# Performance work log

Hardware: AMD Instinct MI355X
Metric: run time of the kernel (lower is better)

## Reference

```python
import jax, jax.numpy as jnp
import numpy as np
from jax import lax

# Geometry constants (mirror ParallelGeometry with angle_ratio=1.0)
PHI_SIZE = 720
T_SIZE = 1024
N = 256            # reco_shape
B = 16             # batch
RHO = float(np.sqrt(2.0))          # ||max_pt - min_pt||/2 for [-1,1]^2
DT = 2.0 * RHO / T_SIZE            # detector step
A = -RHO                           # left edge used in phase factor
DPHI = np.pi / PHI_SIZE            # mean angle step (angle_ratio=1)


def setup_inputs() -> dict:
    key = jax.random.key(0)
    k1, k2, k3 = jax.random.split(key, 3)
    sinos = jax.random.normal(k1, (B, PHI_SIZE, T_SIZE), dtype=jnp.float32)
    kernel_re = jax.random.normal(k2, (T_SIZE // 2 + 1,), dtype=jnp.float32)
    kernel_im = jax.random.normal(k3, (T_SIZE // 2 + 1,), dtype=jnp.float32)
    return {"sinos": sinos, "kernel_re": kernel_re, "kernel_im": kernel_im}


def _filter_sinos(sinos, kernel):
    # fourier_transform (no padding): dt * exp(-i a w) * rfft(sinos)
    omgs = 2.0 * np.pi * jnp.fft.rfftfreq(T_SIZE, d=DT).astype(jnp.float32)  # [T/2+1]
    phase = jnp.exp(-1j * (A * omgs))          # cos(a w) - i sin(a w)
    sino_hat = (DT * phase) * jnp.fft.rfft(sinos, axis=-1)
    filtered_hat = kernel * sino_hat
    # inverse_fourier_transform: exp(+i a w)/dt * filtered_hat, then irfft
    back = (jnp.conj(phase) / DT) * filtered_hat
    return jnp.fft.irfft(back, n=T_SIZE, axis=-1)   # [B, phi, T], real


def _backproject(filtered):
    # Parallel-beam backprojection (ODL RayTransform adjoint):
    # f(x,y) = dphi * sum_phi lin_interp(g[phi], t = x cos(phi) + y sin(phi))
    angles = ((jnp.arange(PHI_SIZE, dtype=jnp.float32) + 0.5) * (np.pi / PHI_SIZE))
    xs = (-1.0 + (jnp.arange(N, dtype=jnp.float32) + 0.5) * (2.0 / N))  # pixel centers
    X, Y = jnp.meshgrid(xs, xs, indexing='ij')      # ODL axis order: [x, y]
    g_seq = jnp.transpose(filtered, (1, 0, 2))      # [phi, B, T]

    def step(acc, inp):
        g, phi = inp                                # g: [B, T]
        t = X * jnp.cos(phi) + Y * jnp.sin(phi)     # [N, N], always in [-rho, rho]
        u = (t + RHO) / DT - 0.5                    # fractional detector index
        i0 = jnp.clip(jnp.floor(u).astype(jnp.int32), 0, T_SIZE - 2)
        w = u - i0.astype(jnp.float32)
        val = g[:, i0] * (1.0 - w) + g[:, i0 + 1] * w   # [B, N, N]
        return acc + val, None

    acc0 = jnp.zeros((filtered.shape[0], N, N), dtype=filtered.dtype)
    acc, _ = lax.scan(step, acc0, (g_seq, angles))
    return acc * jnp.asarray(DPHI, dtype=filtered.dtype)


def reference(sinos, kernel_re, kernel_im):
    kernel = kernel_re.astype(jnp.complex64) + 1j * kernel_im.astype(jnp.complex64)
    filtered = _filter_sinos(sinos, kernel)
    return _backproject(filtered)
```

## Files before the change

kernel.cpp:

```cpp
#include <hip/hip_runtime.h>

#define PHI 720
#define TS 1024
#define NB 16
#define NPIX 256

#define INVDT 362.03867196751236f
#define DXF 0.0078125f
#define DPHI_F 0.0043633231299858237f

#define WS_TW 0
#define WS_ANG 4096
#define WS_PT 8192
#define WS_NEEDED (8192 + 256 * 360 * 16)

__device__ __forceinline__ float2 cmulf2(float2 a, float2 b) {
    return make_float2(a.x * b.x - a.y * b.y, a.x * b.y + a.y * b.x);
}
__device__ __forceinline__ float fract_fast(float x) {
#if __has_builtin(__builtin_amdgcn_fractf)
    return __builtin_amdgcn_fractf(x);
#else
    return x - floorf(x);
#endif
}

__global__ __launch_bounds__(256) void precompute_kernel(char* __restrict__ wsb) {
    const int blk = blockIdx.x, tid = threadIdx.x;
    if (blk < 360) {
        const int e = blk * 256 + tid;
        const unsigned repu = (unsigned)e / 360u;
        const int rep = (int)repu;
        const int a = e - rep * 360;
        const int ti = rep >> 4, tj = rep & 15;
        float s, c;
        sincosf(((float)a + 0.5f) * (3.14159265358979323846f / 720.0f), &s, &c);
        const float x0 = -1.0f + ((float)(ti * 8) + 0.5f) * DXF;
        const float x7 = x0 + 7.0f * DXF;
        const float y0 = -1.0f + ((float)(tj * 8) + 0.5f) * DXF;
        const float y7 = y0 + 7.0f * DXF;
        const float uTmin = (c * x0 + s * y0) * INVDT + 511.5f;
        const float uTmax = (c * x7 + s * y7) * INVDT + 511.5f;
        const float uUmin = (s * x0 - c * y7) * INVDT + 511.5f;
        const float uUmax = (s * x7 - c * y0) * INVDT + 511.5f;
        int wbA = (int)floorf(uTmin - 0.02f) - 1;
        int wbB = (int)floorf(1023.0f - uTmax - 0.02f) - 1;
        int wbC = (int)floorf(uUmin - 0.02f) - 1;
        int wbD = (int)floorf(1023.0f - uUmax - 0.02f) - 1;
        wbA = min(max(wbA, 0), 992);
        wbB = min(max(wbB, 0), 992);
        wbC = min(max(wbC, 0), 992);
        wbD = min(max(wbD, 0), 992);
        uint4 ent;
        ent.x = __float_as_uint(511.5f - (float)wbA);
        ent.y = __float_as_uint(511.5f - (float)wbC);
        ent.z = (unsigned)wbA | ((unsigned)wbB << 16);
        ent.w = (unsigned)wbC | ((unsigned)wbD << 16);
        ((uint4*)(wsb + WS_PT))[e] = ent;
    } else if (blk < 362) {
        const int k = (blk - 360) * 256 + tid;
        float s, c;
        sincosf((float)k * (6.28318530717958647692f / 1024.0f), &s, &c);
        ((float2*)(wsb + WS_TW))[k] = make_float2(c, -s);
    } else {
        const int a = (blk - 362) * 256 + tid;
        if (a < 360) {
            float s, c;
            sincosf(((float)a + 0.5f) * (3.14159265358979323846f / 720.0f), &s, &c);
            ((float2*)(wsb + WS_ANG))[a] = make_float2(c * INVDT, s * INVDT);
        }
    }
}

__device__ __forceinline__ void r4_stage(const float2* __restrict__ s0, float2* __restrict__ d0,
                                         const float2* __restrict__ s1, float2* __restrict__ d1,
                                         const float2* __restrict__ tw, int tid, int m, bool inv) {
    const int q = tid & ~(m - 1);
    const int o = tid + 3 * q;
    float2 w1 = tw[q], w2 = tw[2 * q];
    if (inv) { w1.y = -w1.y; w2.y = -w2.y; }
    #pragma unroll
    for (int f = 0; f < 2; ++f) {
        const float2* s = f ? s1 : s0;
        float2* d = f ? d1 : d0;
        const float2 a = s[tid], b = s[tid + 256], c = s[tid + 512], e = s[tid + 768];
        const float2 A = make_float2(a.x + c.x, a.y + c.y);
        const float2 Bm = cmulf2(w1, make_float2(a.x - c.x, a.y - c.y));
        const float2 C = make_float2(b.x + e.x, b.y + e.y);
        const float2 Dm = cmulf2(w1, make_float2(b.x - e.x, b.y - e.y));
        const float2 D = inv ? make_float2(-Dm.y, Dm.x) : make_float2(Dm.y, -Dm.x);
        d[o]         = make_float2(A.x + C.x, A.y + C.y);
        d[o + m]     = make_float2(Bm.x + D.x, Bm.y + D.y);
        d[o + 2 * m] = cmulf2(w2, make_float2(A.x - C.x, A.y - C.y));
        d[o + 3 * m] = cmulf2(w2, make_float2(Bm.x - D.x, Bm.y - D.y));
    }
}

__device__ __forceinline__ float2 kfac(const float* __restrict__ kr,
                                       const float* __restrict__ ki, int k, float scale) {
    const int kk = (k <= 512) ? k : (1024 - k);
    const float re = kr[kk] * scale;
    float im = ((k == 0) || (k == 512)) ? 0.0f : ki[kk] * scale;
    if (k > 512) im = -im;
    return make_float2(re, im);
}

__global__ __launch_bounds__(256) void filter_fft_kernel(float* __restrict__ sinos,
                                                         const float* __restrict__ kr,
                                                         const float* __restrict__ ki,
                                                         const char* __restrict__ wsb) {
    __shared__ float2 bufA[2][1024];
    __shared__ float2 bufB[2][1024];
    __shared__ float2 tw[512];
    const int tid = threadIdx.x;
    const int wg = blockIdx.x;
    const int lb = (wg & 7) * 360 + (wg >> 3);
    float* base = sinos + (size_t)lb * 4096;

    #pragma unroll
    for (int f = 0; f < 2; ++f) {
        float* r0 = base + f * 2048;
        float* r1 = r0 + 1024;
        #pragma unroll
        for (int h = 0; h < 4; ++h) {
            const int k = tid + h * 256;
            bufA[f][k] = make_float2(r0[k], r1[k]);
        }
    }
    if (wsb) {
        const float2* tg = (const float2*)(wsb + WS_TW);
        tw[tid] = tg[tid];
        tw[tid + 256] = tg[tid + 256];
    } else {
        #pragma unroll
        for (int h = 0; h < 2; ++h) {
            const int k = tid + h * 256;
            float s, c;
            sincosf((float)k * (6.28318530717958647692f / 1024.0f), &s, &c);
            tw[k] = make_float2(c, -s);
        }
    }
    __syncthreads();

    r4_stage(bufA[0], bufB[0], bufA[1], bufB[1], tw, tid, 1, false);   __syncthreads();
    r4_stage(bufB[0], bufA[0], bufB[1], bufA[1], tw, tid, 4, false);   __syncthreads();
    r4_stage(bufA[0], bufB[0], bufA[1], bufB[1], tw, tid, 16, false);  __syncthreads();
    r4_stage(bufB[0], bufA[0], bufB[1], bufA[1], tw, tid, 64, false);  __syncthreads();
    r4_stage(bufA[0], bufB[0], bufA[1], bufB[1], tw, tid, 256, false); __syncthreads();

    {
        const float scale = DPHI_F / 1024.0f;
        const int q = tid;
        const int o = 4 * tid;
        float2 w1 = tw[q], w2 = tw[2 * q];
        w1.y = -w1.y; w2.y = -w2.y;
        const float2 f0 = kfac(kr, ki, tid, scale);
        const float2 f1 = kfac(kr, ki, tid + 256, scale);
        const float2 f2 = kfac(kr, ki, tid + 512, scale);
        const float2 f3 = kfac(kr, ki, tid + 768, scale);
        #pragma unroll
        for (int f = 0; f < 2; ++f) {
            const float2* s = bufB[f];
            float2* d = bufA[f];
            const float2 a = cmulf2(f0, s[tid]);
            const float2 b = cmulf2(f1, s[tid + 256]);
            const float2 c = cmulf2(f2, s[tid + 512]);
            const float2 e = cmulf2(f3, s[tid + 768]);
            const float2 A = make_float2(a.x + c.x, a.y + c.y);
            const float2 Bm = cmulf2(w1, make_float2(a.x - c.x, a.y - c.y));
            const float2 C = make_float2(b.x + e.x, b.y + e.y);
            const float2 Dm = cmulf2(w1, make_float2(b.x - e.x, b.y - e.y));
            const float2 D = make_float2(-Dm.y, Dm.x);
            d[o]     = make_float2(A.x + C.x, A.y + C.y);
            d[o + 1] = make_float2(Bm.x + D.x, Bm.y + D.y);
            d[o + 2] = cmulf2(w2, make_float2(A.x - C.x, A.y - C.y));
            d[o + 3] = cmulf2(w2, make_float2(Bm.x - D.x, Bm.y - D.y));
        }
    }
    __syncthreads();

    r4_stage(bufA[0], bufB[0], bufA[1], bufB[1], tw, tid, 4, true);   __syncthreads();
    r4_stage(bufB[0], bufA[0], bufB[1], bufA[1], tw, tid, 16, true);  __syncthreads();
    r4_stage(bufA[0], bufB[0], bufA[1], bufB[1], tw, tid, 64, true);  __syncthreads();
    r4_stage(bufB[0], bufA[0], bufB[1], bufA[1], tw, tid, 256, true); __syncthreads();

    #pragma unroll
    for (int f = 0; f < 2; ++f) {
        float* r0 = base + f * 2048;
        float* r1 = r0 + 1024;
        #pragma unroll
        for (int h = 0; h < 4; ++h) {
            const int k = tid + h * 256;
            const float2 v = bufA[f][k];
            r0[k] = v.x;
            r1[k] = v.y;
        }
    }
}

__global__ __launch_bounds__(128, 8) void backproj_sym_kernel(const float* __restrict__ filt,
                                                              float* __restrict__ out,
                                                              const char* __restrict__ wsb) {
    __shared__ float lds[2048];
    const int tid = threadIdx.x;
    const int hf = __builtin_amdgcn_readfirstlane(tid >> 6);
    const int l = tid & 63;
    const int wg = blockIdx.x;
    const int lb = ((wg & 7) << 9) | (wg >> 3);
    const int b = lb >> 8;
    const int rep = lb & 255;
    const int ti = rep >> 4, tj = rep & 15;

    const float2* __restrict__ ang = (const float2*)(wsb + WS_ANG);
    const uint4* __restrict__ pt = ((const uint4*)(wsb + WS_PT)) + rep * 360;

    const int ii = l >> 3, jj = l & 7;
    const int ip = ti * 8 + ii, jp = tj * 8 + jj;
    const float Xc = -1.0f + ((float)ip + 0.5f) * DXF;
    const float Yc = -1.0f + ((float)jp + 0.5f) * DXF;
    const int vbyte = ((l & 31) + ((l >> 5) * (360 * 1024))) * 4;
    const float* __restrict__ gb = filt + (size_t)b * (PHI * TS);
    const int lbase = hf * 1024;

    float a0 = 0.f, a1 = 0.f, a2 = 0.f, a3 = 0.f;
    float pf[2][4];

#define STAGE(CH) { \
    _Pragma("unroll") \
    for (int p = 0; p < 2; ++p) { \
        const int ap = hf * 180 + (CH) * 2 + p; \
        const uint4 e = pt[ap]; \
        const char* rp = (const char*)(gb + (ap << 10)); \
        pf[p][0] = *(const float*)(rp + ((e.z & 0xFFFFu) << 2) + vbyte); \
        pf[p][1] = *(const float*)(rp + ((e.z >> 16) << 2) + vbyte); \
        pf[p][2] = *(const float*)(rp + ((e.w & 0xFFFFu) << 2) + vbyte); \
        pf[p][3] = *(const float*)(rp + ((e.w >> 16) << 2) + vbyte); \
    } }

#define WRITE(BUF) { \
    _Pragma("unroll") \
    for (int p = 0; p < 2; ++p) { \
        _Pragma("unroll") \
        for (int w = 0; w < 4; ++w) \
            lds[lbase + (BUF) * 512 + p * 256 + w * 64 + l] = pf[p][w]; \
    } }

#define COMPUTE(BUF, CH) { \
    _Pragma("unroll") \
    for (int p = 0; p < 2; ++p) { \
        const int ap = hf * 180 + (CH) * 2 + p; \
        const uint4 e = pt[ap]; \
        const float2 cs = ang[ap]; \
        const float* slot = &lds[lbase + (BUF) * 512 + p * 256]; \
        const float kFA = __uint_as_float(e.x), kFC = __uint_as_float(e.y); \
        const int wbA = (int)(e.z & 0xFFFFu), wbB = (int)(e.z >> 16); \
        const int wbC = (int)(e.w & 0xFFFFu), wbD = (int)(e.w >> 16); \
        const float uT = fmaf(cs.x, Xc, fmaf(cs.y, Yc, kFA)); \
        const float uU = fmaf(cs.y, Xc, fmaf(cs.x, -Yc, kFC)); \
        const int iA = (int)uT; const float wT = fract_fast(uT); const float oT = 1.0f - wT; \
        const int iC = (int)uU; const float wU = fract_fast(uU); const float oU = 1.0f - wU; \
        const int iB = 1022 - wbA - wbB - iA; \
        const int iD = 1022 - wbC - wbD - iC; \
        { const float g0 = slot[iA],       g1 = slot[iA + 1]; \
          const float h0 = slot[iA + 32],  h1 = slot[iA + 33]; \
          a0 = fmaf(g0, oT, a0); a0 = fmaf(g1, wT, a0); \
          a1 = fmaf(h0, oT, a1); a1 = fmaf(h1, wT, a1); } \
        { const float g0 = slot[64 + iB],  g1 = slot[65 + iB]; \
          const float h0 = slot[96 + iB],  h1 = slot[97 + iB]; \
          a2 = fmaf(g1, oT, a2); a2 = fmaf(g0, wT, a2); \
          a3 = fmaf(h1, oT, a3); a3 = fmaf(h0, wT, a3); } \
        { const float g0 = slot[128 + iC], g1 = slot[129 + iC]; \
          const float h0 = slot[160 + iC], h1 = slot[161 + iC]; \
          a1 = fmaf(g0, oU, a1); a1 = fmaf(g1, wU, a1); \
          a2 = fmaf(h0, oU, a2); a2 = fmaf(h1, wU, a2); } \
        { const float g0 = slot[192 + iD], g1 = slot[193 + iD]; \
          const float h0 = slot[224 + iD], h1 = slot[225 + iD]; \
          a3 = fmaf(g1, oU, a3); a3 = fmaf(g0, wU, a3); \
          a0 = fmaf(h1, oU, a0); a0 = fmaf(h0, wU, a0); } \
    } }

    STAGE(0); WRITE(0);
    for (int cc = 0; cc < 44; ++cc) {
        STAGE(2 * cc + 1);
        COMPUTE(0, 2 * cc);
        WRITE(1);
        STAGE(2 * cc + 2);
        COMPUTE(1, 2 * cc + 1);
        WRITE(0);
    }
    STAGE(89);
    COMPUTE(0, 88);
    WRITE(1);
    COMPUTE(1, 89);

#undef STAGE
#undef WRITE
#undef COMPUTE

    const int bb = b << 8;
    atomicAdd(&out[((size_t)((bb + ip) << 8)) + jp], a0);
    atomicAdd(&out[((size_t)((bb + 255 - jp) << 8)) + ip], a1);
    atomicAdd(&out[((size_t)((bb + 255 - ip) << 8)) + (255 - jp)], a2);
    atomicAdd(&out[((size_t)((bb + jp) << 8)) + (255 - ip)], a3);
}

__global__ __launch_bounds__(256) void backproj_fb_kernel(const float* __restrict__ filt,
                                                          float* __restrict__ out) {
    __shared__ float2 csI[PHI];
    __shared__ float win[8 * 128];
    __shared__ float woffF[8];

    const int tid = threadIdx.x;
    const int wg = blockIdx.x;
    const int lb = ((wg & 7) << 7) | (wg >> 3);
    const int b = lb >> 6;
    const int tile = lb & 63;
    const int i0 = (tile >> 3) * 32;
    const int j0 = (tile & 7) * 32;

    for (int p = tid; p < PHI; p += 256) {
        const float angv = ((float)p + 0.5f) * (float)(3.14159265358979323846 / 720.0);
        float s, c;
        sincosf(angv, &s, &c);
        csI[p] = make_float2(c * INVDT, s * INVDT);
    }

    const int lane = tid & 63;
    const int wv = tid >> 6;
    const int ii = lane & 7;
    const int jj = lane >> 3;
    const int ipx = i0 + ii;
    const int j = j0 + wv * 8 + jj;

    const float Xc = -1.0f + ((float)ipx + 0.5f) * DXF;
    const float Yc = -1.0f + ((float)j + 0.5f) * DXF;

    const int r = tid >> 5;
    const int l32 = tid & 31;
    const float xlo = -1.0f + ((float)i0 + 0.5f) * DXF;
    const float xhi = -1.0f + ((float)i0 + 31.5f) * DXF;
    const float ylo = -1.0f + ((float)j0 + 0.5f) * DXF;
    const float yhi = -1.0f + ((float)j0 + 31.5f) * DXF;

    const float* gb = filt + (size_t)b * PHI * TS;
    float acc0 = 0.f, acc1 = 0.f, acc2 = 0.f, acc3 = 0.f;

    __syncthreads();

    {
        const float2 cs = csI[r];
        const float um = fminf(cs.x * xlo, cs.x * xhi) + fminf(cs.y * ylo, cs.y * yhi) + 511.5f;
        const int wb = (int)floorf(um) - 1;
        const float* grow = gb + (size_t)r * TS;
        #pragma unroll
        for (int h = 0; h < 4; ++h) {
            int gi = wb + l32 + 32 * h;
            gi = gi < 0 ? 0 : (gi > TS - 1 ? TS - 1 : gi);
            win[r * 128 + l32 + 32 * h] = grow[gi];
        }
        if (l32 == 0) woffF[r] = 511.5f + (float)(r * 128 - wb);
    }
    __syncthreads();

    for (int c = 0; c < PHI / 8; ++c) {
        float gp0 = 0.f, gp1 = 0.f, gp2 = 0.f, gp3 = 0.f;
        int wbn = 0;
        const bool more = (c + 1 < PHI / 8);
        if (more) {
            const int a = (c + 1) * 8 + r;
            const float2 cs = csI[a];
            const float um = fminf(cs.x * xlo, cs.x * xhi) + fminf(cs.y * ylo, cs.y * yhi) + 511.5f;
            wbn = (int)floorf(um) - 1;
            const float* grow = gb + (size_t)a * TS;
            int g0 = wbn + l32;      g0 = g0 < 0 ? 0 : (g0 > TS - 1 ? TS - 1 : g0);
            int g1 = wbn + l32 + 32; g1 = g1 < 0 ? 0 : (g1 > TS - 1 ? TS - 1 : g1);
            int g2 = wbn + l32 + 64; g2 = g2 < 0 ? 0 : (g2 > TS - 1 ? TS - 1 : g2);
            int g3 = wbn + l32 + 96; g3 = g3 < 0 ? 0 : (g3 > TS - 1 ? TS - 1 : g3);
            gp0 = grow[g0]; gp1 = grow[g1]; gp2 = grow[g2]; gp3 = grow[g3];
        }
        #pragma unroll
        for (int aa = 0; aa < 8; ++aa) {
            const float2 cs = csI[c * 8 + aa];
            const float offF = woffF[aa];
            float u = fmaf(cs.y, Yc, cs.x * Xc) + offF;
            const float dup = cs.x * 0.0625f;
            #pragma unroll
            for (int p = 0; p < 4; ++p) {
                const int idx = (int)u;
                const float wf = fract_fast(u);
                const float g0 = win[idx], g1 = win[idx + 1];
                if (p == 0) acc0 = fmaf(wf, g1 - g0, acc0 + g0);
                else if (p == 1) acc1 = fmaf(wf, g1 - g0, acc1 + g0);
                else if (p == 2) acc2 = fmaf(wf, g1 - g0, acc2 + g0);
                else acc3 = fmaf(wf, g1 - g0, acc3 + g0);
                u += dup;
            }
        }
        __syncthreads();
        if (more) {
            win[r * 128 + l32] = gp0;
            win[r * 128 + l32 + 32] = gp1;
            win[r * 128 + l32 + 64] = gp2;
            win[r * 128 + l32 + 96] = gp3;
            if (l32 == 0) woffF[r] = 511.5f + (float)(r * 128 - wbn);
        }
        __syncthreads();
    }

    const size_t ob = ((size_t)(b * NPIX + ipx)) * NPIX + j;
    out[ob] = acc0;
    out[ob + 8 * NPIX] = acc1;
    out[ob + 16 * NPIX] = acc2;
    out[ob + 24 * NPIX] = acc3;
}

extern "C" void kernel_launch(void* const* d_in, const int* in_sizes, int n_in,
                              void* d_out, int out_size, void* d_ws, size_t ws_size,
                              hipStream_t stream) {
    float* sinos = (float*)d_in[0];
    const float* kr = (const float*)d_in[1];
    const float* ki = (const float*)d_in[2];
    float* out = (float*)d_out;

    char* wsb = nullptr;
    if (ws_size >= (size_t)WS_NEEDED && d_ws != nullptr) {
        wsb = (char*)d_ws;
        precompute_kernel<<<364, 256, 0, stream>>>(wsb);
    }
    filter_fft_kernel<<<NB * PHI / 4, 256, 0, stream>>>(sinos, kr, ki, wsb);
    if (wsb) {
        hipMemsetAsync(d_out, 0, (size_t)out_size * sizeof(float), stream);
        backproj_sym_kernel<<<4096, 128, 0, stream>>>(sinos, out, wsb);
    } else {
        backproj_fb_kernel<<<NB * 64, 256, 0, stream>>>(sinos, out);
    }
}
```

Baseline: 265.1 us.

## Fuse FFT load/store stages, pad LDS, replace atomics with in-block reduction

The FFT kernel now does the first radix-4 stage directly from global loads and the last inverse stage directly into global stores, which removes two LDS passes and two barriers. It also pads the shared buffers with an index swizzle to cut bank conflicts. The backprojection kernel reduces its two half-waves' partial sums through LDS and writes each output once, so the output memset and global atomics can be dropped. It also splits the accumulators into two parity sets to shorten FMA dependency chains. This relies on each block owning its output pixels exclusively, and it adds one extra barrier per block.

```diff
diff --git a/kernel.cpp b/kernel.cpp
--- a/kernel.cpp
+++ b/kernel.cpp
@@ -13,6 +13,8 @@
 #define WS_ANG 4096
 #define WS_PT 8192
 #define WS_NEEDED (8192 + 256 * 360 * 16)
+
+#define FSW(i) ((i) + ((i) >> 4))
 
 __device__ __forceinline__ float2 cmulf2(float2 a, float2 b) {
     return make_float2(a.x * b.x - a.y * b.y, a.x * b.y + a.y * b.x);
@@ -72,9 +74,9 @@
     }
 }
 
-__device__ __forceinline__ void r4_stage(const float2* __restrict__ s0, float2* __restrict__ d0,
-                                         const float2* __restrict__ s1, float2* __restrict__ d1,
-                                         const float2* __restrict__ tw, int tid, int m, bool inv) {
+__device__ __forceinline__ void r4_sw(const float2* __restrict__ s0, float2* __restrict__ d0,
+                                      const float2* __restrict__ s1, float2* __restrict__ d1,
+                                      const float2* __restrict__ tw, int tid, int m, bool inv) {
     const int q = tid & ~(m - 1);
     const int o = tid + 3 * q;
     float2 w1 = tw[q], w2 = tw[2 * q];
@@ -83,16 +85,17 @@
     for (int f = 0; f < 2; ++f) {
         const float2* s = f ? s1 : s0;
         float2* d = f ? d1 : d0;
-        const float2 a = s[tid], b = s[tid + 256], c = s[tid + 512], e = s[tid + 768];
+        const float2 a = s[FSW(tid)], b = s[FSW(tid + 256)];
+        const float2 c = s[FSW(tid + 512)], e = s[FSW(tid + 768)];
         const float2 A = make_float2(a.x + c.x, a.y + c.y);
         const float2 Bm = cmulf2(w1, make_float2(a.x - c.x, a.y - c.y));
         const float2 C = make_float2(b.x + e.x, b.y + e.y);
         const float2 Dm = cmulf2(w1, make_float2(b.x - e.x, b.y - e.y));
         const float2 D = inv ? make_float2(-Dm.y, Dm.x) : make_float2(Dm.y, -Dm.x);
-        d[o]         = make_float2(A.x + C.x, A.y + C.y);
-        d[o + m]     = make_float2(Bm.x + D.x, Bm.y + D.y);
-        d[o + 2 * m] = cmulf2(w2, make_float2(A.x - C.x, A.y - C.y));
-        d[o + 3 * m] = cmulf2(w2, make_float2(Bm.x - D.x, Bm.y - D.y));
+        d[FSW(o)]         = make_float2(A.x + C.x, A.y + C.y);
+        d[FSW(o + m)]     = make_float2(Bm.x + D.x, Bm.y + D.y);
+        d[FSW(o + 2 * m)] = cmulf2(w2, make_float2(A.x - C.x, A.y - C.y));
+        d[FSW(o + 3 * m)] = cmulf2(w2, make_float2(Bm.x - D.x, Bm.y - D.y));
     }
 }
 
@@ -109,28 +112,21 @@
                                                          const float* __restrict__ kr,
                                                          const float* __restrict__ ki,
                                                          const char* __restrict__ wsb) {
-    __shared__ float2 bufA[2][1024];
-    __shared__ float2 bufB[2][1024];
+    __shared__ float2 bufA[2][1088];
+    __shared__ float2 bufB[2][1088];
     __shared__ float2 tw[512];
     const int tid = threadIdx.x;
     const int wg = blockIdx.x;
     const int lb = (wg & 7) * 360 + (wg >> 3);
     float* base = sinos + (size_t)lb * 4096;
 
-    #pragma unroll
-    for (int f = 0; f < 2; ++f) {
-        float* r0 = base + f * 2048;
-        float* r1 = r0 + 1024;
-        #pragma unroll
-        for (int h = 0; h < 4; ++h) {
-            const int k = tid + h * 256;
-            bufA[f][k] = make_float2(r0[k], r1[k]);
-        }
-    }
+    float2 w1f, w2f;
     if (wsb) {
         const float2* tg = (const float2*)(wsb + WS_TW);
         tw[tid] = tg[tid];
         tw[tid + 256] = tg[tid + 256];
+        w1f = tg[tid];
+        w2f = tg[2 * tid];
     } else {
         #pragma unroll
         for (int h = 0; h < 2; ++h) {
@@ -139,20 +135,43 @@
             sincosf((float)k * (6.28318530717958647692f / 1024.0f), &s, &c);
             tw[k] = make_float2(c, -s);
         }
+        float s, c;
+        sincosf((float)tid * (6.28318530717958647692f / 1024.0f), &s, &c);
+        w1f = make_float2(c, -s);
+        sincosf((float)(2 * tid) * (6.28318530717958647692f / 1024.0f), &s, &c);
+        w2f = make_float2(c, -s);
+    }
+
+    #pragma unroll
+    for (int f = 0; f < 2; ++f) {
+        const float* r0 = base + f * 2048;
+        const float* r1 = r0 + 1024;
+        const float2 a = make_float2(r0[tid], r1[tid]);
+        const float2 b = make_float2(r0[tid + 256], r1[tid + 256]);
+        const float2 c = make_float2(r0[tid + 512], r1[tid + 512]);
+        const float2 e = make_float2(r0[tid + 768], r1[tid + 768]);
+        const float2 A = make_float2(a.x + c.x, a.y + c.y);
+        const float2 Bm = cmulf2(w1f, make_float2(a.x - c.x, a.y - c.y));
+        const float2 C = make_float2(b.x + e.x, b.y + e.y);
+        const float2 Dm = cmulf2(w1f, make_float2(b.x - e.x, b.y - e.y));
+        const float2 D = make_float2(Dm.y, -Dm.x);
+        const int o = 4 * tid;
+        bufA[f][FSW(o)]     = make_float2(A.x + C.x, A.y + C.y);
+        bufA[f][FSW(o + 1)] = make_float2(Bm.x + D.x, Bm.y + D.y);
+        bufA[f][FSW(o + 2)] = cmulf2(w2f, make_float2(A.x - C.x, A.y - C.y));
+        bufA[f][FSW(o + 3)] = cmulf2(w2f, make_float2(Bm.x - D.x, Bm.y - D.y));
     }
     __syncthreads();
 
-    r4_stage(bufA[0], bufB[0], bufA[1], bufB[1], tw, tid, 1, false);   __syncthreads();
-    r4_stage(bufB[0], bufA[0], bufB[1], bufA[1], tw, tid, 4, false);   __syncthreads();
-    r4_stage(bufA[0], bufB[0], bufA[1], bufB[1], tw, tid, 16, false);  __syncthreads();
-    r4_stage(bufB[0], bufA[0], bufB[1], bufA[1], tw, tid, 64, false);  __syncthreads();
-    r4_stage(bufA[0], bufB[0], bufA[1], bufB[1], tw, tid, 256, false); __syncthreads();
+    r4_sw(bufA[0], bufB[0], bufA[1], bufB[1], tw, tid, 4, false);   __syncthreads();
+    r4_sw(bufB[0], bufA[0], bufB[1], bufA[1], tw, tid, 16, false);  __syncthreads();
+    r4_sw(bufA[0], bufB[0], bufA[1], bufB[1], tw, tid, 64, false);  __syncthreads();
+    r4_sw(bufB[0], bufA[0], bufB[1], bufA[1], tw, tid, 256, false); __syncthreads();
 
     {
         const float scale = DPHI_F / 1024.0f;
-        const int q = tid;
         const int o = 4 * tid;
-        float2 w1 = tw[q], w2 = tw[2 * q];
+        float2 w1 = tw[tid], w2 = tw[2 * tid];
         w1.y = -w1.y; w2.y = -w2.y;
         const float2 f0 = kfac(kr, ki, tid, scale);
         const float2 f1 = kfac(kr, ki, tid + 256, scale);
@@ -160,48 +179,52 @@
         const float2 f3 = kfac(kr, ki, tid + 768, scale);
         #pragma unroll
         for (int f = 0; f < 2; ++f) {
-            const float2* s = bufB[f];
-            float2* d = bufA[f];
-            const float2 a = cmulf2(f0, s[tid]);
-            const float2 b = cmulf2(f1, s[tid + 256]);
-            const float2 c = cmulf2(f2, s[tid + 512]);
-            const float2 e = cmulf2(f3, s[tid + 768]);
+            const float2* s = bufA[f];
+            float2* d = bufB[f];
+            const float2 a = cmulf2(f0, s[FSW(tid)]);
+            const float2 b = cmulf2(f1, s[FSW(tid + 256)]);
+            const float2 c = cmulf2(f2, s[FSW(tid + 512)]);
+            const float2 e = cmulf2(f3, s[FSW(tid + 768)]);
             const float2 A = make_float2(a.x + c.x, a.y + c.y);
             const float2 Bm = cmulf2(w1, make_float2(a.x - c.x, a.y - c.y));
             const float2 C = make_float2(b.x + e.x, b.y + e.y);
             const float2 Dm = cmulf2(w1, make_float2(b.x - e.x, b.y - e.y));
             const float2 D = make_float2(-Dm.y, Dm.x);
-            d[o]     = make_float2(A.x + C.x, A.y + C.y);
-            d[o + 1] = make_float2(Bm.x + D.x, Bm.y + D.y);
-            d[o + 2] = cmulf2(w2, make_float2(A.x - C.x, A.y - C.y));
-            d[o + 3] = cmulf2(w2, make_float2(Bm.x - D.x, Bm.y - D.y));
+            d[FSW(o)]     = make_float2(A.x + C.x, A.y + C.y);
+            d[FSW(o + 1)] = make_float2(Bm.x + D.x, Bm.y + D.y);
+            d[FSW(o + 2)] = cmulf2(w2, make_float2(A.x - C.x, A.y - C.y));
+            d[FSW(o + 3)] = cmulf2(w2, make_float2(Bm.x - D.x, Bm.y - D.y));
         }
     }
     __syncthreads();
 
-    r4_stage(bufA[0], bufB[0], bufA[1], bufB[1], tw, tid, 4, true);   __syncthreads();
-    r4_stage(bufB[0], bufA[0], bufB[1], bufA[1], tw, tid, 16, true);  __syncthreads();
-    r4_stage(bufA[0], bufB[0], bufA[1], bufB[1], tw, tid, 64, true);  __syncthreads();
-    r4_stage(bufB[0], bufA[0], bufB[1], bufA[1], tw, tid, 256, true); __syncthreads();
+    r4_sw(bufB[0], bufA[0], bufB[1], bufA[1], tw, tid, 4, true);   __syncthreads();
+    r4_sw(bufA[0], bufB[0], bufA[1], bufB[1], tw, tid, 16, true);  __syncthreads();
+    r4_sw(bufB[0], bufA[0], bufB[1], bufA[1], tw, tid, 64, true);  __syncthreads();
 
     #pragma unroll
     for (int f = 0; f < 2; ++f) {
+        const float2* s = bufA[f];
         float* r0 = base + f * 2048;
         float* r1 = r0 + 1024;
-        #pragma unroll
-        for (int h = 0; h < 4; ++h) {
-            const int k = tid + h * 256;
-            const float2 v = bufA[f][k];
-            r0[k] = v.x;
-            r1[k] = v.y;
-        }
+        const float2 a = s[FSW(tid)], b = s[FSW(tid + 256)];
+        const float2 c = s[FSW(tid + 512)], e = s[FSW(tid + 768)];
+        const float2 A = make_float2(a.x + c.x, a.y + c.y);
+        const float2 Bm = make_float2(a.x - c.x, a.y - c.y);
+        const float2 C = make_float2(b.x + e.x, b.y + e.y);
+        const float2 Dm = make_float2(b.x - e.x, b.y - e.y);
+        const float2 D = make_float2(-Dm.y, Dm.x);
+        r0[tid]       = A.x + C.x;  r1[tid]       = A.y + C.y;
+        r0[tid + 256] = Bm.x + D.x; r1[tid + 256] = Bm.y + D.y;
+        r0[tid + 512] = A.x - C.x;  r1[tid + 512] = A.y - C.y;
+        r0[tid + 768] = Bm.x - D.x; r1[tid + 768] = Bm.y - D.y;
     }
 }
 
 __global__ __launch_bounds__(128, 8) void backproj_sym_kernel(const float* __restrict__ filt,
                                                               float* __restrict__ out,
                                                               const char* __restrict__ wsb) {
-    __shared__ float lds[2048];
+    __shared__ float lds[2304];
     const int tid = threadIdx.x;
     const int hf = __builtin_amdgcn_readfirstlane(tid >> 6);
     const int l = tid & 63;
@@ -222,7 +245,7 @@
     const float* __restrict__ gb = filt + (size_t)b * (PHI * TS);
     const int lbase = hf * 1024;
 
-    float a0 = 0.f, a1 = 0.f, a2 = 0.f, a3 = 0.f;
+    float aP[2][4] = {{0.f, 0.f, 0.f, 0.f}, {0.f, 0.f, 0.f, 0.f}};
     float pf[2][4];
 
 #define STAGE(CH) { \
@@ -263,20 +286,20 @@
         const int iD = 1022 - wbC - wbD - iC; \
         { const float g0 = slot[iA],       g1 = slot[iA + 1]; \
           const float h0 = slot[iA + 32],  h1 = slot[iA + 33]; \
-          a0 = fmaf(g0, oT, a0); a0 = fmaf(g1, wT, a0); \
-          a1 = fmaf(h0, oT, a1); a1 = fmaf(h1, wT, a1); } \
+          aP[p][0] = fmaf(g0, oT, aP[p][0]); aP[p][0] = fmaf(g1, wT, aP[p][0]); \
+          aP[p][1] = fmaf(h0, oT, aP[p][1]); aP[p][1] = fmaf(h1, wT, aP[p][1]); } \
         { const float g0 = slot[64 + iB],  g1 = slot[65 + iB]; \
           const float h0 = slot[96 + iB],  h1 = slot[97 + iB]; \
-          a2 = fmaf(g1, oT, a2); a2 = fmaf(g0, wT, a2); \
-          a3 = fmaf(h1, oT, a3); a3 = fmaf(h0, wT, a3); } \
+          aP[p][2] = fmaf(g1, oT, aP[p][2]); aP[p][2] = fmaf(g0, wT, aP[p][2]); \
+          aP[p][3] = fmaf(h1, oT, aP[p][3]); aP[p][3] = fmaf(h0, wT, aP[p][3]); } \
         { const float g0 = slot[128 + iC], g1 = slot[129 + iC]; \
           const float h0 = slot[160 + iC], h1 = slot[161 + iC]; \
-          a1 = fmaf(g0, oU, a1); a1 = fmaf(g1, wU, a1); \
-          a2 = fmaf(h0, oU, a2); a2 = fmaf(h1, wU, a2); } \
+          aP[p][1] = fmaf(g0, oU, aP[p][1]); aP[p][1] = fmaf(g1, wU, aP[p][1]); \
+          aP[p][2] = fmaf(h0, oU, aP[p][2]); aP[p][2] = fmaf(h1, wU, aP[p][2]); } \
         { const float g0 = slot[192 + iD], g1 = slot[193 + iD]; \
           const float h0 = slot[224 + iD], h1 = slot[225 + iD]; \
-          a3 = fmaf(g1, oU, a3); a3 = fmaf(g0, wU, a3); \
-          a0 = fmaf(h1, oU, a0); a0 = fmaf(h0, wU, a0); } \
+          aP[p][3] = fmaf(g1, oU, aP[p][3]); aP[p][3] = fmaf(g0, wU, aP[p][3]); \
+          aP[p][0] = fmaf(h1, oU, aP[p][0]); aP[p][0] = fmaf(h0, wU, aP[p][0]); } \
     } }
 
     STAGE(0); WRITE(0);
@@ -297,11 +320,24 @@
 #undef WRITE
 #undef COMPUTE
 
-    const int bb = b << 8;
-    atomicAdd(&out[((size_t)((bb + ip) << 8)) + jp], a0);
-    atomicAdd(&out[((size_t)((bb + 255 - jp) << 8)) + ip], a1);
-    atomicAdd(&out[((size_t)((bb + 255 - ip) << 8)) + (255 - jp)], a2);
-    atomicAdd(&out[((size_t)((bb + jp) << 8)) + (255 - ip)], a3);
+    const float s0 = aP[0][0] + aP[1][0];
+    const float s1 = aP[0][1] + aP[1][1];
+    const float s2 = aP[0][2] + aP[1][2];
+    const float s3 = aP[0][3] + aP[1][3];
+    if (hf == 1) {
+        lds[2048 + (l << 2) + 0] = s0;
+        lds[2048 + (l << 2) + 1] = s1;
+        lds[2048 + (l << 2) + 2] = s2;
+        lds[2048 + (l << 2) + 3] = s3;
+    }
+    __syncthreads();
+    if (hf == 0) {
+        const int bb = b << 8;
+        out[((size_t)((bb + ip) << 8)) + jp]               = s0 + lds[2048 + (l << 2) + 0];
+        out[((size_t)((bb + 255 - jp) << 8)) + ip]         = s1 + lds[2048 + (l << 2) + 1];
+        out[((size_t)((bb + 255 - ip) << 8)) + (255 - jp)] = s2 + lds[2048 + (l << 2) + 2];
+        out[((size_t)((bb + jp) << 8)) + (255 - ip)]       = s3 + lds[2048 + (l << 2) + 3];
+    }
 }
 
 __global__ __launch_bounds__(256) void backproj_fb_kernel(const float* __restrict__ filt,
@@ -429,7 +465,6 @@
     }
     filter_fft_kernel<<<NB * PHI / 4, 256, 0, stream>>>(sinos, kr, ki, wsb);
     if (wsb) {
-        hipMemsetAsync(d_out, 0, (size_t)out_size * sizeof(float), stream);
         backproj_sym_kernel<<<4096, 128, 0, stream>>>(sinos, out, wsb);
     } else {
         backproj_fb_kernel<<<NB * 64, 256, 0, stream>>>(sinos, out);
```

Result: faster. 251.9 us (-5.0%).
